# Optimization experiments

Hardware: AMD Instinct MI355X
Metric: run time of the kernel (lower is better)

The kernel has to match this reference:

```python
import jax, jax.numpy as jnp
import numpy as np

M1 = M2 = M3 = 8  # retained modes per spatial dim


def get_3d_clifford_kernel(w, g):
    # w: (8, O, I, 2m1, 2m2, 2m3); returns (8O, 8I, 2m1, 2m2, 2m3)
    g0, g1, g2 = g[0], g[1], g[2]
    k0 = jnp.concatenate([w[0], w[1] * g0, w[2] * g1, w[3] * g2, -w[4] * g0 * g1, -w[5] * g0 * g2, -w[6] * g1 * g2, -w[7] * g0 * g1 * g2], axis=1)
    k1 = jnp.concatenate([w[1], w[0], -w[4] * g1, -w[5] * g2, w[2] * g1, w[3] * g2, -w[7] * g1 * g2, -w[6] * g1 * g2], axis=1)
    k2 = jnp.concatenate([w[2], w[4] * g0, w[0], -w[6] * g2, -w[1] * g0, w[7] * g0 * g2, w[3] * g2, w[5] * g0 * g2], axis=1)
    k3 = jnp.concatenate([w[3], w[5] * g0, w[6] * g1, w[0], -w[7] * g0 * g1, -w[1] * g0, -w[2] * g1, -w[4] * g0 * g1], axis=1)
    k4 = jnp.concatenate([w[4], w[2], -w[1], g2 * w[7], w[0], -w[6] * g2, w[5] * g2, w[3] * g2], axis=1)
    k5 = jnp.concatenate([w[5], w[3], -w[7] * g1, -w[1], w[6] * g1, w[0], -w[4] * g1, -w[2] * g1], axis=1)
    k6 = jnp.concatenate([w[6], w[7] * g0, w[3], -w[2], -w[5] * g0, w[4] * g0, w[0], w[1] * g0], axis=1)
    k7 = jnp.concatenate([w[7], w[6], -w[5], w[4], w[3], -w[2], w[1], w[0]], axis=1)
    return jnp.concatenate([k0, k1, k2, k3, k4, k5, k6, k7], axis=0)


def setup_inputs() -> dict:
    key = jax.random.key(0)
    k1, k2 = jax.random.split(key)
    B, D, H, W, Cin, Cout = 4, 48, 48, 48, 24, 24
    x = jax.random.normal(k1, (B, D, H, W, Cin, 8), dtype=jnp.float32)
    scale = 1.0 / (Cin * Cout)
    weights = scale * jax.random.uniform(k2, (8, Cout, Cin, 2 * M1, 2 * M2, 2 * M3), dtype=jnp.float32)
    return {"x": x, "weights": weights}


def reference(x, weights):
    B, D, H, W, Cin, _ = x.shape
    Cout = weights.shape[1]
    g = jnp.ones(3, dtype=x.dtype)  # metric (1, 1, 1)
    # complex-dual packing of the 8 blades
    d1 = x[..., 0] + 1j * x[..., 7]
    d2 = x[..., 1] + 1j * x[..., 6]
    d3 = x[..., 2] + 1j * x[..., 5]
    d4 = x[..., 3] + 1j * x[..., 4]
    f1 = jnp.fft.fftn(d1, axes=(1, 2, 3))
    f2 = jnp.fft.fftn(d2, axes=(1, 2, 3))
    f3 = jnp.fft.fftn(d3, axes=(1, 2, 3))
    f4 = jnp.fft.fftn(d4, axes=(1, 2, 3))
    bchw = lambda t: t.transpose(0, 4, 1, 2, 3)
    # (B, 8*Cin, D, H, W) real tensor of blade spectra
    mv_ft = jnp.concatenate([bchw(f1.real), bchw(f2.real), bchw(f3.real), bchw(f4.real),
                             bchw(f4.imag), bchw(f3.imag), bchw(f2.imag), bchw(f1.imag)], axis=1)
    # gather the 8 low/high-frequency octant corners -> (B, 8Cin, 2m1, 2m2, 2m3)
    i1 = jnp.concatenate([jnp.arange(M1), jnp.arange(D - M1, D)])
    i2 = jnp.concatenate([jnp.arange(M2), jnp.arange(H - M2, H)])
    i3 = jnp.concatenate([jnp.arange(M3), jnp.arange(W - M3, W)])
    input_mul = mv_ft[:, :, i1[:, None, None], i2[None, :, None], i3[None, None, :]]
    kernel = get_3d_clifford_kernel(weights, g)  # (8Cout, 8Cin, 2m1, 2m2, 2m3)
    output_mul = jnp.einsum("bixyz,oixyz->boxyz", input_mul, kernel)
    # scatter back to full spectrum
    out_ft = jnp.zeros((B, 8 * Cout, D, H, W), dtype=mv_ft.dtype)
    out_ft = out_ft.at[:, :, i1[:, None, None], i2[None, :, None], i3[None, None, :]].set(output_mul)
    out_ft = out_ft.reshape(B, 8, Cout, D, H, W).transpose(0, 2, 3, 4, 5, 1)  # (B, Cout, D, H, W, 8)
    o1 = out_ft[..., 0] + 1j * out_ft[..., 7]
    o2 = out_ft[..., 1] + 1j * out_ft[..., 6]
    o3 = out_ft[..., 2] + 1j * out_ft[..., 5]
    o4 = out_ft[..., 3] + 1j * out_ft[..., 4]
    g1_ = jnp.fft.ifftn(o1, axes=(2, 3, 4))
    g2_ = jnp.fft.ifftn(o2, axes=(2, 3, 4))
    g3_ = jnp.fft.ifftn(o3, axes=(2, 3, 4))
    g4_ = jnp.fft.ifftn(o4, axes=(2, 3, 4))
    output = jnp.stack([g1_.real, g2_.real, g3_.real, g4_.real,
                        g4_.imag, g3_.imag, g2_.imag, g1_.imag], axis=-1)  # (B, Cout, D, H, W, 8)
    return output.transpose(0, 2, 3, 4, 1, 5)  # (B, D, H, W, Cout, 8)
```

## Files before the change

kernel.cpp:

```cpp
#include <hip/hip_runtime.h>
#include <math.h>


#define C866 0.8660254037844386f

constexpr float FC0[8] = {1.0f, 0.99144486137885f, 0.96592582628907f, 0.92387953251129f,
                          0.86602540378444f, 0.79335334029124f, 0.70710678118655f, 0.60876142900872f};
constexpr float FS0[8] = {0.0f, 0.13052619222005f, 0.25881904510252f, 0.38268343236509f,
                          0.5f, 0.60876142900872f, 0.70710678118655f, 0.79335334029124f};
constexpr float FC1[8] = {0.5f, 0.60876142900872f, 0.70710678118655f, 0.79335334029124f,
                          0.86602540378444f, 0.92387953251129f, 0.96592582628907f, 0.99144486137885f};
constexpr float FS1[8] = {-0.86602540378444f, -0.79335334029124f, -0.70710678118655f, -0.60876142900872f,
                          -0.5f, -0.38268343236509f, -0.25881904510252f, -0.13052619222005f};

__device__ __forceinline__ uint32_t c2h(float2 z) {
  union { _Float16 h[2]; uint32_t u; } v;
  v.h[0] = (_Float16)z.x; v.h[1] = (_Float16)z.y;
  return v.u;
}
__device__ __forceinline__ float2 h2c(uint32_t u) {
  union { uint32_t u; _Float16 h[2]; } v;
  v.u = u;
  return make_float2((float)v.h[0], (float)v.h[1]);
}

__device__ __forceinline__ float2 cmul(float2 a, float2 b) {
  return make_float2(fmaf(a.x, b.x, -(a.y * b.y)), fmaf(a.x, b.y, a.y * b.x));
}
__device__ __forceinline__ void cfma(float2& acc, float2 a, float2 t) {
  acc.x = fmaf(a.x, t.x, acc.x); acc.x = fmaf(-a.y, t.y, acc.x);
  acc.y = fmaf(a.x, t.y, acc.y); acc.y = fmaf(a.y, t.x, acc.y);
}

struct FwdState {
  float2 acc[8], t[8], stp[8];
  float2 R1, R2;
};

__device__ __forceinline__ void fwd_init(FwdState& st, int half) {
#pragma unroll
  for (int r = 0; r < 8; ++r) {
    st.acc[r] = make_float2(0.f, 0.f);
    st.t[r] = make_float2(1.f, 0.f);
    st.stp[r] = make_float2(half ? FC1[r] : FC0[r],
                            half ? -FS1[r] : -FS0[r]);
  }
  st.R1 = half ? make_float2(-0.5f, -C866) : make_float2(1.f, 0.f);
  st.R2 = half ? make_float2(-0.5f,  C866) : make_float2(1.f, 0.f);
}

__device__ __forceinline__ void fwd_stepf(FwdState& st, float2 z0, float2 z1, float2 z2) {
  z1 = cmul(z1, st.R1);
  z2 = cmul(z2, st.R2);
  const float sx = z1.x + z2.x, sy = z1.y + z2.y;
  const float dx = z1.x - z2.x, dy = z1.y - z2.y;
  const float2 y0 = make_float2(z0.x + sx, z0.y + sy);
  const float tx = fmaf(-0.5f, sx, z0.x), ty = fmaf(-0.5f, sy, z0.y);
  const float ex = C866 * dx, ey = C866 * dy;
  const float2 y1 = make_float2(tx + ey, ty - ex);
  const float2 y2 = make_float2(tx - ey, ty + ex);
#pragma unroll
  for (int r = 0; r < 8; ++r) {
    const float2 yy = (r % 3 == 0) ? y0 : ((r % 3 == 1) ? y1 : y2);
    cfma(st.acc[r], yy, st.t[r]);
    st.t[r] = cmul(st.t[r], st.stp[r]);
  }
}

struct InvState {
  float2 zr[16], t[16];
};

__device__ __forceinline__ void inv_init(InvState& st) {
#pragma unroll
  for (int m = 0; m < 16; ++m) st.t[m] = make_float2(1.f, 0.f);
}

__device__ __forceinline__ void inv_stepf(InvState& st, float2& o0, float2& o1, float2& o2) {
  constexpr int JG[16] = {0,1,2,0,1,2,0,1, 1,2,0,1,2,0,1,2};
  float2 u0 = make_float2(0.f, 0.f), u1 = u0, u2 = u0;
#pragma unroll
  for (int m = 0; m < 16; ++m) {
    float2& uu = (JG[m] == 0) ? u0 : ((JG[m] == 1) ? u1 : u2);
    cfma(uu, st.zr[m], st.t[m]);
    const float2 stp = (m < 8) ? make_float2(FC0[m], FS0[m])
                               : make_float2(FC1[m - 8], FS1[m - 8]);
    st.t[m] = cmul(st.t[m], stp);
  }
  const float sx = u1.x + u2.x, sy = u1.y + u2.y;
  const float dx = u1.x - u2.x, dy = u1.y - u2.y;
  o0 = make_float2(u0.x + sx, u0.y + sy);
  const float tx = fmaf(-0.5f, sx, u0.x), ty = fmaf(-0.5f, sy, u0.y);
  const float ex = C866 * dx, ey = C866 * dy;
  o1 = make_float2(tx - ey, ty + ex);
  o2 = make_float2(tx + ey, ty - ex);
}

__global__ __launch_bounds__(192) void k_fwd_w(const float* __restrict__ x,
                                               uint32_t* __restrict__ A) {
  __shared__ __align__(16) uint32_t xs[48 * 96];
  {
    const float* xp = x + (size_t)blockIdx.x * 9216;
    for (int idx = threadIdx.x; idx < 1152; idx += 192) {
      const int w = idx / 24, ci = idx % 24;
      const float4 u = *(const float4*)(xp + w * 192 + ci * 8);
      const float4 v = *(const float4*)(xp + w * 192 + ci * 8 + 4);
      uint4 d;
      d.x = c2h(make_float2(u.x, v.w));
      d.y = c2h(make_float2(u.y, v.z));
      d.z = c2h(make_float2(u.z, v.y));
      d.w = c2h(make_float2(u.w, v.x));
      *(uint4*)(&xs[w * 96 + ci * 4]) = d;
    }
  }
  __syncthreads();

  const int q = threadIdx.x % 96, half = threadIdx.x / 96;
  FwdState st;
  fwd_init(st, half);
#pragma unroll 4
  for (int j = 0; j < 16; ++j) {
    const float2 z0 = h2c(xs[j * 96 + q]);
    const float2 z1 = h2c(xs[(j + 16) * 96 + q]);
    const float2 z2 = h2c(xs[(j + 32) * 96 + q]);
    fwd_stepf(st, z0, z1, z2);
  }
  uint32_t* Ap = A + (size_t)blockIdx.x * 1536 + q;
#pragma unroll
  for (int r = 0; r < 8; ++r) Ap[(half * 8 + r) * 96] = c2h(st.acc[r]);
}

__global__ __launch_bounds__(192) void k_fwd_h(const uint32_t* __restrict__ A,
                                               uint32_t* __restrict__ Bv) {
  const int k3 = blockIdx.x & 15, bd = blockIdx.x >> 4;
  const int q = threadIdx.x % 96, half = threadIdx.x / 96;
  const uint32_t* Ap = A + ((size_t)bd * 768 + k3) * 96 + q;
  FwdState st;
  fwd_init(st, half);
  for (int j = 0; j < 16; ++j) {
    const float2 z0 = h2c(Ap[(size_t)j * 1536]);
    const float2 z1 = h2c(Ap[(size_t)(j + 16) * 1536]);
    const float2 z2 = h2c(Ap[(size_t)(j + 32) * 1536]);
    fwd_stepf(st, z0, z1, z2);
  }
  uint32_t* Bp = Bv + ((size_t)bd * 256 + k3) * 96 + q;
#pragma unroll
  for (int r = 0; r < 8; ++r) Bp[(size_t)(half * 8 + r) * 1536] = c2h(st.acc[r]);
}

__global__ __launch_bounds__(192) void k_fwd_d(const uint32_t* __restrict__ Bv,
                                               float2* __restrict__ Cv) {
  const int k23 = blockIdx.x & 255, b = blockIdx.x >> 8;
  const int q = threadIdx.x % 96, half = threadIdx.x / 96;
  const uint32_t* Bp = Bv + ((size_t)b * 12288 + k23) * 96 + q;
  FwdState st;
  fwd_init(st, half);
  for (int j = 0; j < 16; ++j) {
    const float2 z0 = h2c(Bp[(size_t)j * 24576]);
    const float2 z1 = h2c(Bp[(size_t)(j + 16) * 24576]);
    const float2 z2 = h2c(Bp[(size_t)(j + 32) * 24576]);
    fwd_stepf(st, z0, z1, z2);
  }
  float2* Cp = Cv + ((size_t)b * 4096 + k23) * 96 + q;
#pragma unroll
  for (int r = 0; r < 8; ++r) Cp[(size_t)(half * 8 + r) * 24576] = st.acc[r];
}

__global__ __launch_bounds__(512) void k_einsum(const float2* __restrict__ Cv,
                                                const float* __restrict__ wgt,
                                                float2* __restrict__ OMz) {
  const int lane = threadIdx.x & 63;
  const int mode = blockIdx.x * 64 + lane;
  const int sub = threadIdx.x >> 6;
  const int col = sub & 3;
  const int cih = sub >> 2;
  const int co = blockIdx.y * 4 + col;
  const int ci0 = cih * 12;

  constexpr int WIDX[8][8] = {
      {0, 1, 2, 3, 4, 5, 6, 7}, {1, 0, 4, 5, 2, 3, 7, 6},
      {2, 4, 0, 6, 1, 7, 3, 5}, {3, 5, 6, 0, 7, 1, 2, 4},
      {4, 2, 1, 7, 0, 6, 5, 3}, {5, 3, 7, 1, 6, 0, 4, 2},
      {6, 7, 3, 2, 5, 4, 0, 1}, {7, 6, 5, 4, 3, 2, 1, 0}};
  constexpr int SGN[8][8] = {
      {1, 1, 1, 1, -1, -1, -1, -1}, {1, 1, -1, -1, 1, 1, -1, -1},
      {1, 1, 1, -1, -1, 1, 1, 1},   {1, 1, 1, 1, -1, -1, -1, -1},
      {1, 1, -1, 1, 1, -1, 1, 1},   {1, 1, -1, -1, 1, 1, -1, -1},
      {1, 1, 1, -1, -1, 1, 1, 1},   {1, 1, -1, 1, 1, -1, 1, 1}};

  float acc[8][4];
#pragma unroll
  for (int bo = 0; bo < 8; ++bo)
#pragma unroll
    for (int b = 0; b < 4; ++b) acc[bo][b] = 0.f;

  for (int ci = ci0; ci < ci0 + 12; ++ci) {
    float w8[8];
#pragma unroll
    for (int k = 0; k < 8; ++k)
      w8[k] = wgt[(size_t)((k * 24 + co) * 24 + ci) * 4096 + mode];
#pragma unroll
    for (int b = 0; b < 4; ++b) {
      const float4* cp =
          (const float4*)(Cv + ((size_t)(b * 4096 + mode) * 96 + ci * 4));
      const float4 u = cp[0], v = cp[1];
      const float inv[8] = {u.x, u.z, v.x, v.z, v.w, v.y, u.w, u.y};
#pragma unroll
      for (int bo = 0; bo < 8; ++bo) {
#pragma unroll
        for (int bi = 0; bi < 8; ++bi) {
          const float wv = w8[WIDX[bo][bi]];
          if (SGN[bo][bi] > 0)
            acc[bo][b] = fmaf(wv, inv[bi], acc[bo][b]);
          else
            acc[bo][b] = fmaf(wv, -inv[bi], acc[bo][b]);
        }
      }
    }
  }

  __shared__ float red[32][4][64];
  if (cih == 1) {
#pragma unroll
    for (int bo = 0; bo < 8; ++bo)
#pragma unroll
      for (int b = 0; b < 4; ++b) red[bo * 4 + b][col][lane] = acc[bo][b];
  }
  __syncthreads();
  if (cih == 0) {
#pragma unroll
    for (int bo = 0; bo < 8; ++bo)
#pragma unroll
      for (int b = 0; b < 4; ++b) acc[bo][b] += red[bo * 4 + b][col][lane];
#pragma unroll
    for (int b = 0; b < 4; ++b) {
      float2* op = OMz + ((size_t)(b * 4096 + mode) * 96 + co * 4);
#pragma unroll
      for (int c = 0; c < 4; ++c) op[c] = make_float2(acc[c][b], acc[7 - c][b]);
    }
  }
}

__global__ __launch_bounds__(192) void k_inv_d(const float2* __restrict__ OMz,
                                               uint32_t* __restrict__ IS1) {
  const int col = blockIdx.x * 2 + threadIdx.x / 96;
  const int q = threadIdx.x % 96;
  const int k23 = col & 255, b = col >> 8;
  InvState st;
#pragma unroll
  for (int m = 0; m < 16; ++m)
    st.zr[m] = OMz[((size_t)b * 4096 + m * 256 + k23) * 96 + q];
  inv_init(st);
  uint32_t* Op = IS1 + ((size_t)b * 12288 + k23) * 96 + q;
  for (int j = 0; j < 16; ++j) {
    float2 o0, o1, o2;
    inv_stepf(st, o0, o1, o2);
    Op[(size_t)j * 24576] = c2h(o0);
    Op[(size_t)(j + 16) * 24576] = c2h(o1);
    Op[(size_t)(j + 32) * 24576] = c2h(o2);
  }
}

__global__ __launch_bounds__(192) void k_inv_h(const uint32_t* __restrict__ IS1,
                                               uint32_t* __restrict__ IS2) {
  const int col = blockIdx.x * 2 + threadIdx.x / 96;
  const int q = threadIdx.x % 96;
  const int m3 = col & 15, bd = col >> 4;
  InvState st;
#pragma unroll
  for (int m = 0; m < 16; ++m)
    st.zr[m] = h2c(IS1[((size_t)bd * 256 + m * 16 + m3) * 96 + q]);
  inv_init(st);
  uint32_t* Op = IS2 + ((size_t)bd * 768 + m3) * 96 + q;
  for (int j = 0; j < 16; ++j) {
    float2 o0, o1, o2;
    inv_stepf(st, o0, o1, o2);
    Op[(size_t)j * 1536] = c2h(o0);
    Op[(size_t)(j + 16) * 1536] = c2h(o1);
    Op[(size_t)(j + 32) * 1536] = c2h(o2);
  }
}

__global__ __launch_bounds__(192) void k_inv_w(const uint32_t* __restrict__ IS2,
                                               float* __restrict__ out) {
  const int blk = blockIdx.x * 2 + threadIdx.x / 96;
  const int q = threadIdx.x % 96;
  const int co = q >> 2, c = q & 3;
  const float norm = 1.0f / 110592.0f;
  InvState st;
#pragma unroll
  for (int m = 0; m < 16; ++m) {
    float2 z = h2c(IS2[((size_t)blk * 16 + m) * 96 + q]);
    st.zr[m] = make_float2(z.x * norm, z.y * norm);
  }
  inv_init(st);
  float* ob = out + (size_t)blk * 9216 + co * 8;
  for (int j = 0; j < 16; ++j) {
    float2 o0, o1, o2;
    inv_stepf(st, o0, o1, o2);
    float* p0 = ob + (size_t)j * 192;
    float* p1 = ob + (size_t)(j + 16) * 192;
    float* p2 = ob + (size_t)(j + 32) * 192;
    p0[c] = o0.x; p0[7 - c] = o0.y;
    p1[c] = o1.x; p1[7 - c] = o1.y;
    p2[c] = o2.x; p2[7 - c] = o2.y;
  }
}

extern "C" void kernel_launch(void* const* d_in, const int* in_sizes, int n_in,
                              void* d_out, int out_size, void* d_ws, size_t ws_size,
                              hipStream_t stream) {
  (void)in_sizes; (void)n_in; (void)out_size; (void)ws_size;
  const float* x = (const float*)d_in[0];
  const float* wgt = (const float*)d_in[1];
  float* out = (float*)d_out;

  char* ob = (char*)d_out;
  uint32_t* A   = (uint32_t*)(ob + 0);
  uint32_t* Bv  = (uint32_t*)(ob + 56623104);
  float2*   Cv  = (float2*)(ob + 75497472);
  float2*   OMz = (float2*)(ob + 88080384);
  uint32_t* IS1 = (uint32_t*)(ob + 0);
  uint32_t* IS2 = (uint32_t*)d_ws;

  k_fwd_w<<<9216, 192, 0, stream>>>(x, A);
  k_fwd_h<<<3072, 192, 0, stream>>>(A, Bv);
  k_fwd_d<<<1024, 192, 0, stream>>>(Bv, Cv);
  k_einsum<<<dim3(64, 6), 512, 0, stream>>>(Cv, wgt, OMz);
  k_inv_d<<<512, 192, 0, stream>>>(OMz, IS1);
  k_inv_h<<<1536, 192, 0, stream>>>(IS1, IS2);
  k_inv_w<<<4608, 192, 0, stream>>>(IS2, out);
}
```

Measured before the change: 361.1 us.

## Store spectral modes in fp16 and drop the ci-split reduction in einsum

```diff
diff --git a/kernel.cpp b/kernel.cpp
--- a/kernel.cpp
+++ b/kernel.cpp
@@ -137,6 +137,7 @@
   const uint32_t* Ap = A + ((size_t)bd * 768 + k3) * 96 + q;
   FwdState st;
   fwd_init(st, half);
+#pragma unroll 4
   for (int j = 0; j < 16; ++j) {
     const float2 z0 = h2c(Ap[(size_t)j * 1536]);
     const float2 z1 = h2c(Ap[(size_t)(j + 16) * 1536]);
@@ -149,33 +150,29 @@
 }
 
 __global__ __launch_bounds__(192) void k_fwd_d(const uint32_t* __restrict__ Bv,
-                                               float2* __restrict__ Cv) {
+                                               uint32_t* __restrict__ Cv) {
   const int k23 = blockIdx.x & 255, b = blockIdx.x >> 8;
   const int q = threadIdx.x % 96, half = threadIdx.x / 96;
   const uint32_t* Bp = Bv + ((size_t)b * 12288 + k23) * 96 + q;
   FwdState st;
   fwd_init(st, half);
+#pragma unroll 4
   for (int j = 0; j < 16; ++j) {
     const float2 z0 = h2c(Bp[(size_t)j * 24576]);
     const float2 z1 = h2c(Bp[(size_t)(j + 16) * 24576]);
     const float2 z2 = h2c(Bp[(size_t)(j + 32) * 24576]);
     fwd_stepf(st, z0, z1, z2);
   }
-  float2* Cp = Cv + ((size_t)b * 4096 + k23) * 96 + q;
-#pragma unroll
-  for (int r = 0; r < 8; ++r) Cp[(size_t)(half * 8 + r) * 24576] = st.acc[r];
-}
-
-__global__ __launch_bounds__(512) void k_einsum(const float2* __restrict__ Cv,
+  uint32_t* Cp = Cv + ((size_t)b * 4096 + k23) * 96 + q;
+#pragma unroll
+  for (int r = 0; r < 8; ++r) Cp[(size_t)(half * 8 + r) * 24576] = c2h(st.acc[r]);
+}
+
+__global__ __launch_bounds__(256) void k_einsum(const uint32_t* __restrict__ Cv,
                                                 const float* __restrict__ wgt,
-                                                float2* __restrict__ OMz) {
-  const int lane = threadIdx.x & 63;
-  const int mode = blockIdx.x * 64 + lane;
-  const int sub = threadIdx.x >> 6;
-  const int col = sub & 3;
-  const int cih = sub >> 2;
-  const int co = blockIdx.y * 4 + col;
-  const int ci0 = cih * 12;
+                                                uint32_t* __restrict__ OMz) {
+  const int mode = blockIdx.x * 64 + (threadIdx.x & 63);
+  const int co = blockIdx.y * 4 + (threadIdx.x >> 6);
 
   constexpr int WIDX[8][8] = {
       {0, 1, 2, 3, 4, 5, 6, 7}, {1, 0, 4, 5, 2, 3, 7, 6},
@@ -194,17 +191,16 @@
 #pragma unroll
     for (int b = 0; b < 4; ++b) acc[bo][b] = 0.f;
 
-  for (int ci = ci0; ci < ci0 + 12; ++ci) {
+  for (int ci = 0; ci < 24; ++ci) {
     float w8[8];
 #pragma unroll
     for (int k = 0; k < 8; ++k)
       w8[k] = wgt[(size_t)((k * 24 + co) * 24 + ci) * 4096 + mode];
 #pragma unroll
     for (int b = 0; b < 4; ++b) {
-      const float4* cp =
-          (const float4*)(Cv + ((size_t)(b * 4096 + mode) * 96 + ci * 4));
-      const float4 u = cp[0], v = cp[1];
-      const float inv[8] = {u.x, u.z, v.x, v.z, v.w, v.y, u.w, u.y};
+      const uint4 U = *(const uint4*)(Cv + ((size_t)(b * 4096 + mode) * 96 + ci * 4));
+      const float2 z0 = h2c(U.x), z1 = h2c(U.y), z2 = h2c(U.z), z3 = h2c(U.w);
+      const float inv[8] = {z0.x, z1.x, z2.x, z3.x, z3.y, z2.y, z1.y, z0.y};
 #pragma unroll
       for (int bo = 0; bo < 8; ++bo) {
 #pragma unroll
@@ -218,30 +214,18 @@
       }
     }
   }
-
-  __shared__ float red[32][4][64];
-  if (cih == 1) {
-#pragma unroll
-    for (int bo = 0; bo < 8; ++bo)
-#pragma unroll
-      for (int b = 0; b < 4; ++b) red[bo * 4 + b][col][lane] = acc[bo][b];
-  }
-  __syncthreads();
-  if (cih == 0) {
-#pragma unroll
-    for (int bo = 0; bo < 8; ++bo)
-#pragma unroll
-      for (int b = 0; b < 4; ++b) acc[bo][b] += red[bo * 4 + b][col][lane];
-#pragma unroll
-    for (int b = 0; b < 4; ++b) {
-      float2* op = OMz + ((size_t)(b * 4096 + mode) * 96 + co * 4);
-#pragma unroll
-      for (int c = 0; c < 4; ++c) op[c] = make_float2(acc[c][b], acc[7 - c][b]);
-    }
-  }
-}
-
-__global__ __launch_bounds__(192) void k_inv_d(const float2* __restrict__ OMz,
+#pragma unroll
+  for (int b = 0; b < 4; ++b) {
+    uint4 P;
+    P.x = c2h(make_float2(acc[0][b], acc[7][b]));
+    P.y = c2h(make_float2(acc[1][b], acc[6][b]));
+    P.z = c2h(make_float2(acc[2][b], acc[5][b]));
+    P.w = c2h(make_float2(acc[3][b], acc[4][b]));
+    *(uint4*)(OMz + ((size_t)(b * 4096 + mode) * 96 + co * 4)) = P;
+  }
+}
+
+__global__ __launch_bounds__(192) void k_inv_d(const uint32_t* __restrict__ OMz,
                                                uint32_t* __restrict__ IS1) {
   const int col = blockIdx.x * 2 + threadIdx.x / 96;
   const int q = threadIdx.x % 96;
@@ -249,9 +233,10 @@
   InvState st;
 #pragma unroll
   for (int m = 0; m < 16; ++m)
-    st.zr[m] = OMz[((size_t)b * 4096 + m * 256 + k23) * 96 + q];
+    st.zr[m] = h2c(OMz[((size_t)b * 4096 + m * 256 + k23) * 96 + q]);
   inv_init(st);
   uint32_t* Op = IS1 + ((size_t)b * 12288 + k23) * 96 + q;
+#pragma unroll 2
   for (int j = 0; j < 16; ++j) {
     float2 o0, o1, o2;
     inv_stepf(st, o0, o1, o2);
@@ -272,6 +257,7 @@
     st.zr[m] = h2c(IS1[((size_t)bd * 256 + m * 16 + m3) * 96 + q]);
   inv_init(st);
   uint32_t* Op = IS2 + ((size_t)bd * 768 + m3) * 96 + q;
+#pragma unroll 2
   for (int j = 0; j < 16; ++j) {
     float2 o0, o1, o2;
     inv_stepf(st, o0, o1, o2);
@@ -295,6 +281,7 @@
   }
   inv_init(st);
   float* ob = out + (size_t)blk * 9216 + co * 8;
+#pragma unroll 2
   for (int j = 0; j < 16; ++j) {
     float2 o0, o1, o2;
     inv_stepf(st, o0, o1, o2);
@@ -318,15 +305,15 @@
   char* ob = (char*)d_out;
   uint32_t* A   = (uint32_t*)(ob + 0);
   uint32_t* Bv  = (uint32_t*)(ob + 56623104);
-  float2*   Cv  = (float2*)(ob + 75497472);
-  float2*   OMz = (float2*)(ob + 88080384);
+  uint32_t* Cv  = (uint32_t*)(ob + 75497472);
+  uint32_t* OMz = (uint32_t*)(ob + 81788928);
   uint32_t* IS1 = (uint32_t*)(ob + 0);
   uint32_t* IS2 = (uint32_t*)d_ws;
 
   k_fwd_w<<<9216, 192, 0, stream>>>(x, A);
   k_fwd_h<<<3072, 192, 0, stream>>>(A, Bv);
   k_fwd_d<<<1024, 192, 0, stream>>>(Bv, Cv);
-  k_einsum<<<dim3(64, 6), 512, 0, stream>>>(Cv, wgt, OMz);
+  k_einsum<<<dim3(64, 6), 256, 0, stream>>>(Cv, wgt, OMz);
   k_inv_d<<<512, 192, 0, stream>>>(OMz, IS1);
   k_inv_h<<<1536, 192, 0, stream>>>(IS1, IS2);
   k_inv_w<<<4608, 192, 0, stream>>>(IS2, out);
```

Measured after the change: 314.2 us. 13.0% less time.
